# Kernel tuning notes

Hardware: AMD Instinct MI355X
Metric: run time of the kernel (lower is better)

The kernel has to match this reference:

```python
import jax, jax.numpy as jnp
import numpy as np

B, L, C, H = 16, 1024, 512, 8
D = C // H
SCALE = D ** -0.5


def setup_inputs() -> dict:
    key = jax.random.key(0)
    ks = jax.random.split(key, 16)
    s = 0.02  # weight init scale
    inp = {
        "query": jax.random.normal(ks[0], (B, L, C), jnp.float32),
        "query_pos": jax.random.normal(ks[1], (B, L, C), jnp.float32),
        "Wqc": jax.random.normal(ks[2], (C, C), jnp.float32) * s,
        "bqc": jax.random.normal(ks[3], (C,), jnp.float32) * s,
        "Wqp": jax.random.normal(ks[4], (C, C), jnp.float32) * s,
        "bqp": jax.random.normal(ks[5], (C,), jnp.float32) * s,
        "Wkc": jax.random.normal(ks[6], (C, C), jnp.float32) * s,
        "bkc": jax.random.normal(ks[7], (C,), jnp.float32) * s,
        "Wkp": jax.random.normal(ks[8], (C, C), jnp.float32) * s,
        "bkp": jax.random.normal(ks[9], (C,), jnp.float32) * s,
        "Wv": jax.random.normal(ks[10], (C, C), jnp.float32) * s,
        "bv": jax.random.normal(ks[11], (C,), jnp.float32) * s,
        "Wo": jax.random.normal(ks[12], (C, C), jnp.float32) * s,
        "bo": jax.random.normal(ks[13], (C,), jnp.float32) * s,
    }
    return inp


def reference(query, query_pos, Wqc, bqc, Wqp, bqp, Wkc, bkc, Wkp, bkp, Wv, bv, Wo, bo):
    # key = query, value = key, identity = query, key_pos = query_pos (shapes match)
    qc = query @ Wqc.T + bqc          # [B, L, C]
    qp = query_pos @ Wqp.T + bqp
    kc = query @ Wkc.T + bkc
    kp = query_pos @ Wkp.T + bkp
    v = query @ Wv.T + bv

    def split_heads(x):  # [B, L, C] -> [B, H, L, D]
        return x.reshape(B, L, H, D).transpose(0, 2, 1, 3)

    q = split_heads(qc + qp) * SCALE
    k = split_heads(kc + kp)
    vh = split_heads(v)

    attn = jnp.einsum("bhqd,bhkd->bhqk", q, k)
    attn = jax.nn.softmax(attn, axis=-1)
    out = jnp.einsum("bhqk,bhkd->bhqd", attn, vh)  # [B, H, L, D]
    out = out.transpose(0, 2, 1, 3).reshape(B, L, C)
    out = out @ Wo.T + bo
    return query + out
```

## Files before the change

kernel.cpp:

```cpp
#include <hip/hip_runtime.h>

typedef __attribute__((ext_vector_type(8))) short short8;
typedef __attribute__((ext_vector_type(4))) short short4v;
typedef __attribute__((ext_vector_type(4))) float f32x4;
typedef unsigned short u16;

#define QSCALE 0.18033688011112042f

#define BB 16
#define LL 1024
#define CC 512
#define HH 8
#define DD 64
#define MROWS (BB*LL)
#define KPROJ 1024
#define NPROJ 1536

#define WS_XCAT   0ull
#define WS_WCAT   (WS_XCAT + (size_t)MROWS*KPROJ*2)
#define WS_WO     (WS_WCAT + (size_t)NPROJ*KPROJ*2)
#define WS_BIAS   (WS_WO   + (size_t)CC*CC*2)
#define WS_QH     (WS_BIAS + 8192)
#define WS_KH     (WS_QH + (size_t)MROWS*CC*2)
#define WS_VT     (WS_KH + (size_t)MROWS*CC*2)
#define WS_OH     (WS_VT + (size_t)MROWS*CC*2)
#define WS_END    (WS_OH + (size_t)MROWS*CC*2)

__device__ inline short f2bf(float f) {
  unsigned u = __builtin_bit_cast(unsigned, f);
  u = (u + 0x7FFFu + ((u >> 16) & 1u)) >> 16;
  return (short)u;
}

__device__ inline short8 pack8(const float* src) {
  float4 a = ((const float4*)src)[0];
  float4 b = ((const float4*)src)[1];
  short8 v;
  v[0]=f2bf(a.x); v[1]=f2bf(a.y); v[2]=f2bf(a.z); v[3]=f2bf(a.w);
  v[4]=f2bf(b.x); v[5]=f2bf(b.y); v[6]=f2bf(b.z); v[7]=f2bf(b.w);
  return v;
}

__device__ inline void gload_lds16(const u16* g, char* lds_byte) {
  __builtin_amdgcn_global_load_lds(
      (const __attribute__((address_space(1))) unsigned int*)g,
      (__attribute__((address_space(3))) unsigned int*)lds_byte,
      16, 0, 0);
}

__global__ __launch_bounds__(256) void pack_all_kernel(
    const float* __restrict__ q, const float* __restrict__ qp,
    const float* __restrict__ Wqc, const float* __restrict__ Wqp,
    const float* __restrict__ Wkc, const float* __restrict__ Wkp,
    const float* __restrict__ Wv,  const float* __restrict__ Wo,
    const float* __restrict__ bqc, const float* __restrict__ bqp,
    const float* __restrict__ bkc, const float* __restrict__ bkp,
    const float* __restrict__ bv,
    u16* __restrict__ xcat, u16* __restrict__ wcat, u16* __restrict__ wo_bf,
    float* __restrict__ bias_cat) {
  if (blockIdx.x < 8192) {
    int o = blockIdx.x * 256 + threadIdx.x;
    int row = o >> 7;
    int kk  = (o & 127) << 3;
    const float* src = (kk < 512) ? (q + (size_t)row * 512 + kk)
                                  : (qp + (size_t)row * 512 + (kk - 512));
    short8 v = pack8(src);
    *(short8*)(xcat + (size_t)row * KPROJ + kk) = v;
    return;
  }
  int o = (blockIdx.x - 8192) * 256 + threadIdx.x;
  if (o < 196608) {
    int j = o >> 7;
    int kk = (o & 127) << 3;
    const float* src = nullptr;
    if (j < 512)        src = (kk < 512) ? Wqc + (size_t)j * 512 + kk : Wqp + (size_t)j * 512 + (kk - 512);
    else if (j < 1024) { int jj = j - 512;  src = (kk < 512) ? Wkc + (size_t)jj * 512 + kk : Wkp + (size_t)jj * 512 + (kk - 512); }
    else               { int jj = j - 1024; src = (kk < 512) ? Wv  + (size_t)jj * 512 + kk : nullptr; }
    short8 v = {0,0,0,0,0,0,0,0};
    if (src) v = pack8(src);
    *(short8*)(wcat + (size_t)j * KPROJ + kk) = v;
  } else if (o < 229376) {
    int o2 = o - 196608;
    int j = o2 >> 6;
    int kk = (o2 & 63) << 3;
    short8 v = pack8(Wo + (size_t)j * 512 + kk);
    *(short8*)(wo_bf + (size_t)j * 512 + kk) = v;
  }
  if (o < 1536) {
    float v;
    if (o < 512)       v = bqc[o] + bqp[o];
    else if (o < 1024) v = bkc[o - 512] + bkp[o - 512];
    else               v = bv[o - 1024];
    bias_cat[o] = v;
  }
}

template <int KDIM>
__device__ inline void gemm128_loop(const u16* __restrict__ A, const u16* __restrict__ Bw,
                                    int m0, int n0, int nt, u16* lds, f32x4 (&acc)[4][4]) {
  const int tid = threadIdx.x;
  const int lane = tid & 63, wave = tid >> 6;
  const int wr = wave >> 1, wc = wave & 1;
  const int lr = lane & 15, lg = lane >> 4;

  auto stage = [&](int buf, int t) {
    int k0 = t * 64;
    #pragma unroll
    for (int i = 0; i < 4; ++i) {
      int s = i * 256 + tid;
      int row = s >> 3, col = s & 7;
      int colp = col ^ (row & 7);
      gload_lds16(A + (size_t)(m0 + row) * KDIM + k0 + colp * 8,
                  (char*)lds + (size_t)buf * 32768 + (size_t)(i * 256 + wave * 64) * 16);
      gload_lds16(Bw + (size_t)(n0 + row) * KDIM + k0 + colp * 8,
                  (char*)lds + (size_t)buf * 32768 + 16384 + (size_t)(i * 256 + wave * 64) * 16);
    }
  };

  auto rdA = [&](int buf, int mf, int ks) {
    int rowl = wr * 64 + mf * 16 + lr;
    int ch = (ks * 4 + lg) ^ (rowl & 7);
    return *(const short8*)(lds + (size_t)buf * 16384 + (size_t)rowl * 64 + ch * 8);
  };
  auto rdB = [&](int buf, int nf, int ks) {
    int rowl = wc * 64 + nf * 16 + lr;
    int ch = (ks * 4 + lg) ^ (rowl & 7);
    return *(const short8*)(lds + (size_t)buf * 16384 + 8192 + (size_t)rowl * 64 + ch * 8);
  };

  stage(0, 0);
  asm volatile("s_waitcnt vmcnt(0)" ::: "memory");
  __builtin_amdgcn_s_barrier();

  int cur = 0;
  for (int t = 0; t < nt; ++t) {
    if (t + 1 < nt) stage(cur ^ 1, t + 1);
    short8 bf[4][2], af[4][2];
    #pragma unroll
    for (int nf = 0; nf < 4; ++nf)
      #pragma unroll
      for (int ks = 0; ks < 2; ++ks) bf[nf][ks] = rdB(cur, nf, ks);
    #pragma unroll
    for (int mf = 0; mf < 4; ++mf)
      #pragma unroll
      for (int ks = 0; ks < 2; ++ks) af[mf][ks] = rdA(cur, mf, ks);
    __builtin_amdgcn_s_setprio(1);
    #pragma unroll
    for (int mf = 0; mf < 4; ++mf)
      #pragma unroll
      for (int nf = 0; nf < 4; ++nf)
        #pragma unroll
        for (int ks = 0; ks < 2; ++ks)
          acc[mf][nf] = __builtin_amdgcn_mfma_f32_16x16x32_bf16(
              bf[nf][ks], af[mf][ks], acc[mf][nf], 0, 0, 0);
    __builtin_amdgcn_s_setprio(0);
    asm volatile("s_waitcnt vmcnt(0)" ::: "memory");
    __builtin_amdgcn_s_barrier();
    cur ^= 1;
  }
}

__global__ __launch_bounds__(256, 2) void proj_gemm_kernel(
    const u16* __restrict__ Xcat, const u16* __restrict__ Wcat,
    const float* __restrict__ bias_cat,
    u16* __restrict__ Qh, u16* __restrict__ Kh, u16* __restrict__ Vt) {
  __shared__ __align__(16) u16 lds[2 * 16384];

  int id0 = blockIdx.x;
  int swz = (id0 & 7) * 192 + (id0 >> 3);
  int bx = swz / 12, by = swz % 12;
  const int m0 = bx * 128, n0 = by * 128;

  const int tid = threadIdx.x;
  const int lane = tid & 63, wave = tid >> 6;
  const int wr = wave >> 1, wc = wave & 1;
  const int lr = lane & 15, lg = lane >> 4;

  f32x4 acc[4][4];
  f32x4 z4 = {0.f, 0.f, 0.f, 0.f};
  #pragma unroll
  for (int mf = 0; mf < 4; ++mf)
    #pragma unroll
    for (int nf = 0; nf < 4; ++nf) acc[mf][nf] = z4;

  const int nt = (n0 >= 1024) ? 8 : 16;
  gemm128_loop<KPROJ>(Xcat, Wcat, m0, n0, nt, lds, acc);

  if (n0 < 1024) {
    const int cbase = n0 + wc * 64 + lg * 4;
    #pragma unroll
    for (int mf = 0; mf < 4; ++mf) {
      int lglob = m0 + wr * 64 + mf * 16 + lr;
      int bidx = lglob >> 10, lrow = lglob & 1023;
      #pragma unroll
      for (int nf = 0; nf < 4; ++nf) {
        int c = cbase + nf * 16;
        float4 bb = *(const float4*)&bias_cat[c];
        int sec = c >> 9, cj = c & 511;
        int h = cj >> 6, d0 = cj & 63;
        size_t idx = ((size_t)(bidx * HH + h) * LL + lrow) * DD + d0;
        float v0 = acc[mf][nf][0] + bb.x;
        float v1 = acc[mf][nf][1] + bb.y;
        float v2 = acc[mf][nf][2] + bb.z;
        float v3 = acc[mf][nf][3] + bb.w;
        if (sec == 0) { v0 *= QSCALE; v1 *= QSCALE; v2 *= QSCALE; v3 *= QSCALE; }
        short4v o;
        o[0] = f2bf(v0); o[1] = f2bf(v1); o[2] = f2bf(v2); o[3] = f2bf(v3);
        u16* dst = (sec == 0) ? Qh : Kh;
        *(short4v*)&dst[idx] = o;
      }
    }
  } else {
    u16* T = lds;
    #pragma unroll
    for (int mf = 0; mf < 4; ++mf) {
      int ll = wr * 64 + mf * 16 + lr;
      #pragma unroll
      for (int nf = 0; nf < 4; ++nf) {
        int cjl = wc * 64 + nf * 16 + lg * 4;
        int c = n0 + cjl;
        float4 bb = *(const float4*)&bias_cat[c];
        T[(size_t)(cjl + 0) * 136 + ll] = (u16)f2bf(acc[mf][nf][0] + bb.x);
        T[(size_t)(cjl + 1) * 136 + ll] = (u16)f2bf(acc[mf][nf][1] + bb.y);
        T[(size_t)(cjl + 2) * 136 + ll] = (u16)f2bf(acc[mf][nf][2] + bb.z);
        T[(size_t)(cjl + 3) * 136 + ll] = (u16)f2bf(acc[mf][nf][3] + bb.w);
      }
    }
    __builtin_amdgcn_s_barrier();
    int b = m0 >> 10, lrow0 = m0 & 1023;
    #pragma unroll
    for (int i = 0; i < 8; ++i) {
      int c2 = i * 256 + tid;
      int r = c2 >> 4;
      int o8 = (c2 & 15) * 8;
      short8 v = *(const short8*)&T[(size_t)r * 136 + o8];
      int cj = n0 - 1024 + r;
      int h = cj >> 6, d = cj & 63;
      *(short8*)&Vt[((size_t)(b * HH + h) * DD + d) * LL + lrow0 + o8] = v;
    }
  }
}

__global__ __launch_bounds__(256, 2) void out_gemm_kernel(
    const u16* __restrict__ Oh, const u16* __restrict__ Wo_bf,
    const float* __restrict__ bo, const float* __restrict__ query,
    float* __restrict__ out) {
  __shared__ __align__(16) u16 lds[2 * 16384];

  int id0 = blockIdx.x;
  int swz = (id0 & 7) * 64 + (id0 >> 3);
  int bx = swz / 4, by = swz % 4;
  const int m0 = bx * 128, n0 = by * 128;

  const int lane = threadIdx.x & 63, wave = threadIdx.x >> 6;
  const int wr = wave >> 1, wc = wave & 1;
  const int lr = lane & 15, lg = lane >> 4;

  f32x4 acc[4][4];
  f32x4 z4 = {0.f, 0.f, 0.f, 0.f};
  #pragma unroll
  for (int mf = 0; mf < 4; ++mf)
    #pragma unroll
    for (int nf = 0; nf < 4; ++nf) acc[mf][nf] = z4;

  gemm128_loop<CC>(Oh, Wo_bf, m0, n0, CC / 64, lds, acc);

  const int cbase = n0 + wc * 64 + lg * 4;
  #pragma unroll
  for (int mf = 0; mf < 4; ++mf) {
    int rw = m0 + wr * 64 + mf * 16 + lr;
    #pragma unroll
    for (int nf = 0; nf < 4; ++nf) {
      int c = cbase + nf * 16;
      float4 bb = *(const float4*)&bo[c];
      size_t idx = (size_t)rw * CC + c;
      float4 qq = *(const float4*)&query[idx];
      float4 o;
      o.x = acc[mf][nf][0] + bb.x + qq.x;
      o.y = acc[mf][nf][1] + bb.y + qq.y;
      o.z = acc[mf][nf][2] + bb.z + qq.z;
      o.w = acc[mf][nf][3] + bb.w + qq.w;
      *(float4*)&out[idx] = o;
    }
  }
}

__global__ __launch_bounds__(256, 2) void attn_kernel(
    const u16* __restrict__ Qh, const u16* __restrict__ Kh,
    const u16* __restrict__ Vt, u16* __restrict__ Oh) {
  __shared__ __align__(16) u16 Kl[2][64 * 64];
  __shared__ __align__(16) u16 Vl[2][64 * 64];
  __shared__ __align__(16) char Pp[4][8192];

  const int tid = threadIdx.x;
  const int lane = tid & 63, wave = tid >> 6;
  const int lr = lane & 15, lg = lane >> 4;
  const int sw = (lr & 7) * 2;
  int n = blockIdx.x;
  int rest = n >> 3;
  const int bh = (n & 7) * 16 + (rest >> 2);
  const int q0 = (rest & 3) * 256;

  const u16* Qb = Qh + (size_t)bh * LL * DD;
  const u16* Kb = Kh + (size_t)bh * LL * DD;
  const u16* Vb = Vt + (size_t)bh * DD * LL;

  short8 aq[4][2];
  #pragma unroll
  for (int m = 0; m < 4; ++m)
    #pragma unroll
    for (int s = 0; s < 2; ++s)
      aq[m][s] = *(const short8*)(Qb + (size_t)(q0 + wave * 64 + m * 16 + lr) * DD + s * 32 + lg * 8);

  f32x4 z4 = {0.f, 0.f, 0.f, 0.f};
  f32x4 oaccT[4][4];
  #pragma unroll
  for (int m = 0; m < 4; ++m)
    #pragma unroll
    for (int db = 0; db < 4; ++db) oaccT[m][db] = z4;
  float lsums[4] = {0.f, 0.f, 0.f, 0.f};

  auto stage = [&](int buf, int kt) {
    int kk0 = kt * 64;
    #pragma unroll
    for (int i = 0; i < 2; ++i) {
      int c = i * 256 + wave * 64 + lane;
      int row = c >> 3, koct = c & 7;
      int ks = koct ^ (row & 7);
      gload_lds16(Kb + (size_t)(kk0 + row) * DD + ks * 8,
                  (char*)&Kl[buf][0] + (size_t)(i * 4 + wave) * 1024);
      gload_lds16(Vb + (size_t)row * LL + kk0 + ks * 8,
                  (char*)&Vl[buf][0] + (size_t)(i * 4 + wave) * 1024);
    }
  };

  stage(0, 0);
  int cur = 0;
  char* Pw = &Pp[wave][0];
  for (int kt = 0; kt < 16; ++kt) {
    if (kt + 1 < 16) {
      stage(cur ^ 1, kt + 1);
      asm volatile("s_waitcnt vmcnt(4)" ::: "memory");
    } else {
      asm volatile("s_waitcnt vmcnt(0)" ::: "memory");
    }
    __builtin_amdgcn_s_barrier();
    __builtin_amdgcn_sched_barrier(0);

    short8 ka[2][4];
    #pragma unroll
    for (int s = 0; s < 2; ++s)
      #pragma unroll
      for (int kb = 0; kb < 4; ++kb) {
        int key = kb * 16 + lr;
        int dct = s * 4 + lg;
        ka[s][kb] = *(const short8*)((const char*)&Kl[cur][0] + (size_t)key * 128 + ((dct ^ (key & 7)) << 4));
      }
    f32x4 ps[4][4];
    #pragma unroll
    for (int m = 0; m < 4; ++m)
      #pragma unroll
      for (int kb = 0; kb < 4; ++kb) ps[m][kb] = z4;
    __builtin_amdgcn_s_setprio(1);
    #pragma unroll
    for (int s = 0; s < 2; ++s)
      #pragma unroll
      for (int kb = 0; kb < 4; ++kb)
        #pragma unroll
        for (int m = 0; m < 4; ++m)
          ps[m][kb] = __builtin_amdgcn_mfma_f32_16x16x32_bf16(ka[s][kb], aq[m][s], ps[m][kb], 0, 0, 0);
    __builtin_amdgcn_s_setprio(0);

    #pragma unroll
    for (int m = 0; m < 4; ++m) {
      #pragma unroll
      for (int kb = 0; kb < 4; ++kb) {
        float p0, p1, p2, p3;
        asm("v_exp_f32 %0, %1" : "=v"(p0) : "v"(ps[m][kb][0]));
        asm("v_exp_f32 %0, %1" : "=v"(p1) : "v"(ps[m][kb][1]));
        asm("v_exp_f32 %0, %1" : "=v"(p2) : "v"(ps[m][kb][2]));
        asm("v_exp_f32 %0, %1" : "=v"(p3) : "v"(ps[m][kb][3]));
        lsums[m] += (p0 + p1) + (p2 + p3);
        unsigned lo, hi;
        asm("v_cvt_pk_bf16_f32 %0, %1, %2" : "=v"(lo) : "v"(p0), "v"(p1));
        asm("v_cvt_pk_bf16_f32 %0, %1, %2" : "=v"(hi) : "v"(p2), "v"(p3));
        uint2 w; w.x = lo; w.y = hi;
        *(uint2*)(Pw + m * 2048 + lr * 128 + ((((kb * 4 + lg) ^ sw)) << 3)) = w;
      }
    }

    short8 bv[2][4];
    #pragma unroll
    for (int s = 0; s < 2; ++s)
      #pragma unroll
      for (int db = 0; db < 4; ++db) {
        int d = db * 16 + lr;
        int kct = s * 4 + lg;
        bv[s][db] = *(const short8*)((const char*)&Vl[cur][0] + (size_t)d * 128 + ((kct ^ (d & 7)) << 4));
      }

    asm volatile("s_waitcnt lgkmcnt(0)" ::: "memory");
    __builtin_amdgcn_sched_barrier(0);

    __builtin_amdgcn_s_setprio(1);
    #pragma unroll
    for (int m = 0; m < 4; ++m) {
      #pragma unroll
      for (int s = 0; s < 2; ++s) {
        int val0 = s * 8 + lg * 2;
        uint4 pw = *(const uint4*)(Pw + m * 2048 + lr * 128 + (((val0 ^ sw)) << 3));
        short8 ap = __builtin_bit_cast(short8, pw);
        #pragma unroll
        for (int db = 0; db < 4; ++db)
          oaccT[m][db] = __builtin_amdgcn_mfma_f32_16x16x32_bf16(bv[s][db], ap, oaccT[m][db], 0, 0, 0);
      }
    }
    __builtin_amdgcn_s_setprio(0);

    __builtin_amdgcn_s_barrier();
    cur ^= 1;
  }

  int b = bh >> 3, h = bh & 7;
  #pragma unroll
  for (int m = 0; m < 4; ++m) {
    float v = lsums[m];
    v += __shfl_xor(v, 16);
    v += __shfl_xor(v, 32);
    float inv = 1.0f / v;
    int q = q0 + wave * 64 + m * 16 + lr;
    #pragma unroll
    for (int db = 0; db < 4; ++db) {
      int d0 = db * 16 + lg * 4;
      short4v o;
      #pragma unroll
      for (int r = 0; r < 4; ++r) o[r] = f2bf(oaccT[m][db][r] * inv);
      *(short4v*)&Oh[(size_t)(b * LL + q) * CC + h * 64 + d0] = o;
    }
  }
}

extern "C" void kernel_launch(void* const* d_in, const int* in_sizes, int n_in,
                              void* d_out, int out_size, void* d_ws, size_t ws_size,
                              hipStream_t stream) {
  (void)in_sizes; (void)n_in; (void)out_size;
  const float* query = (const float*)d_in[0];
  const float* qpos  = (const float*)d_in[1];
  const float* Wqc = (const float*)d_in[2];
  const float* bqc = (const float*)d_in[3];
  const float* Wqp = (const float*)d_in[4];
  const float* bqp = (const float*)d_in[5];
  const float* Wkc = (const float*)d_in[6];
  const float* bkc = (const float*)d_in[7];
  const float* Wkp = (const float*)d_in[8];
  const float* bkp = (const float*)d_in[9];
  const float* Wv  = (const float*)d_in[10];
  const float* bv  = (const float*)d_in[11];
  const float* Wo  = (const float*)d_in[12];
  const float* bo  = (const float*)d_in[13];

  char* ws = (char*)d_ws;
  if (ws_size < WS_END) return;

  u16*   Xcat     = (u16*)(ws + WS_XCAT);
  u16*   Wcat     = (u16*)(ws + WS_WCAT);
  u16*   Wo_bf    = (u16*)(ws + WS_WO);
  float* bias_cat = (float*)(ws + WS_BIAS);
  u16*   Qh       = (u16*)(ws + WS_QH);
  u16*   Kh       = (u16*)(ws + WS_KH);
  u16*   Vtr      = (u16*)(ws + WS_VT);
  u16*   Oh       = (u16*)(ws + WS_OH);
  float* out      = (float*)d_out;

  pack_all_kernel<<<dim3(9088), dim3(256), 0, stream>>>(
      query, qpos, Wqc, Wqp, Wkc, Wkp, Wv, Wo,
      bqc, bqp, bkc, bkp, bv, Xcat, Wcat, Wo_bf, bias_cat);
  proj_gemm_kernel<<<dim3((MROWS / 128) * (NPROJ / 128)), dim3(256), 0, stream>>>(
      Xcat, Wcat, bias_cat, Qh, Kh, Vtr);
  attn_kernel<<<dim3(512), dim3(256), 0, stream>>>(Qh, Kh, Vtr, Oh);
  out_gemm_kernel<<<dim3((MROWS / 128) * (CC / 128)), dim3(256), 0, stream>>>(
      Oh, Wo_bf, bo, query, out);
}
```

Baseline: 145.4 us.

## Halve GEMM K-tile to 32 and raise occupancy to four blocks per CU

```diff
diff --git a/kernel.cpp b/kernel.cpp
--- a/kernel.cpp
+++ b/kernel.cpp
@@ -104,28 +104,28 @@
   const int lr = lane & 15, lg = lane >> 4;
 
   auto stage = [&](int buf, int t) {
-    int k0 = t * 64;
-    #pragma unroll
-    for (int i = 0; i < 4; ++i) {
+    int k0 = t * 32;
+    #pragma unroll
+    for (int i = 0; i < 2; ++i) {
       int s = i * 256 + tid;
-      int row = s >> 3, col = s & 7;
-      int colp = col ^ (row & 7);
+      int row = s >> 2, col = s & 3;
+      int colp = col ^ (row & 3);
       gload_lds16(A + (size_t)(m0 + row) * KDIM + k0 + colp * 8,
-                  (char*)lds + (size_t)buf * 32768 + (size_t)(i * 256 + wave * 64) * 16);
+                  (char*)lds + (size_t)buf * 16384 + (size_t)(i * 256 + wave * 64) * 16);
       gload_lds16(Bw + (size_t)(n0 + row) * KDIM + k0 + colp * 8,
-                  (char*)lds + (size_t)buf * 32768 + 16384 + (size_t)(i * 256 + wave * 64) * 16);
+                  (char*)lds + (size_t)buf * 16384 + 8192 + (size_t)(i * 256 + wave * 64) * 16);
     }
   };
 
-  auto rdA = [&](int buf, int mf, int ks) {
+  auto rdA = [&](int buf, int mf) {
     int rowl = wr * 64 + mf * 16 + lr;
-    int ch = (ks * 4 + lg) ^ (rowl & 7);
-    return *(const short8*)(lds + (size_t)buf * 16384 + (size_t)rowl * 64 + ch * 8);
+    int ch = lg ^ (rowl & 3);
+    return *(const short8*)(lds + (size_t)buf * 8192 + (size_t)rowl * 32 + ch * 8);
   };
-  auto rdB = [&](int buf, int nf, int ks) {
+  auto rdB = [&](int buf, int nf) {
     int rowl = wc * 64 + nf * 16 + lr;
-    int ch = (ks * 4 + lg) ^ (rowl & 7);
-    return *(const short8*)(lds + (size_t)buf * 16384 + 8192 + (size_t)rowl * 64 + ch * 8);
+    int ch = lg ^ (rowl & 3);
+    return *(const short8*)(lds + (size_t)buf * 8192 + 4096 + (size_t)rowl * 32 + ch * 8);
   };
 
   stage(0, 0);
@@ -135,24 +135,18 @@
   int cur = 0;
   for (int t = 0; t < nt; ++t) {
     if (t + 1 < nt) stage(cur ^ 1, t + 1);
-    short8 bf[4][2], af[4][2];
-    #pragma unroll
-    for (int nf = 0; nf < 4; ++nf)
-      #pragma unroll
-      for (int ks = 0; ks < 2; ++ks) bf[nf][ks] = rdB(cur, nf, ks);
+    short8 bf[4], af[4];
+    #pragma unroll
+    for (int nf = 0; nf < 4; ++nf) bf[nf] = rdB(cur, nf);
+    #pragma unroll
+    for (int mf = 0; mf < 4; ++mf) af[mf] = rdA(cur, mf);
+    __builtin_amdgcn_s_setprio(1);
     #pragma unroll
     for (int mf = 0; mf < 4; ++mf)
       #pragma unroll
-      for (int ks = 0; ks < 2; ++ks) af[mf][ks] = rdA(cur, mf, ks);
-    __builtin_amdgcn_s_setprio(1);
-    #pragma unroll
-    for (int mf = 0; mf < 4; ++mf)
-      #pragma unroll
       for (int nf = 0; nf < 4; ++nf)
-        #pragma unroll
-        for (int ks = 0; ks < 2; ++ks)
-          acc[mf][nf] = __builtin_amdgcn_mfma_f32_16x16x32_bf16(
-              bf[nf][ks], af[mf][ks], acc[mf][nf], 0, 0, 0);
+        acc[mf][nf] = __builtin_amdgcn_mfma_f32_16x16x32_bf16(
+            bf[nf], af[mf], acc[mf][nf], 0, 0, 0);
     __builtin_amdgcn_s_setprio(0);
     asm volatile("s_waitcnt vmcnt(0)" ::: "memory");
     __builtin_amdgcn_s_barrier();
@@ -160,11 +154,11 @@
   }
 }
 
-__global__ __launch_bounds__(256, 2) void proj_gemm_kernel(
+__global__ __launch_bounds__(256, 4) void proj_gemm_kernel(
     const u16* __restrict__ Xcat, const u16* __restrict__ Wcat,
     const float* __restrict__ bias_cat,
     u16* __restrict__ Qh, u16* __restrict__ Kh, u16* __restrict__ Vt) {
-  __shared__ __align__(16) u16 lds[2 * 16384];
+  __shared__ __align__(16) u16 lds[2 * 8192];
 
   int id0 = blockIdx.x;
   int swz = (id0 & 7) * 192 + (id0 >> 3);
@@ -183,7 +177,7 @@
     #pragma unroll
     for (int nf = 0; nf < 4; ++nf) acc[mf][nf] = z4;
 
-  const int nt = (n0 >= 1024) ? 8 : 16;
+  const int nt = (n0 >= 1024) ? 16 : 32;
   gemm128_loop<KPROJ>(Xcat, Wcat, m0, n0, nt, lds, acc);
 
   if (n0 < 1024) {
@@ -212,40 +206,46 @@
     }
   } else {
     u16* T = lds;
-    #pragma unroll
-    for (int mf = 0; mf < 4; ++mf) {
-      int ll = wr * 64 + mf * 16 + lr;
-      #pragma unroll
-      for (int nf = 0; nf < 4; ++nf) {
-        int cjl = wc * 64 + nf * 16 + lg * 4;
-        int c = n0 + cjl;
-        float4 bb = *(const float4*)&bias_cat[c];
-        T[(size_t)(cjl + 0) * 136 + ll] = (u16)f2bf(acc[mf][nf][0] + bb.x);
-        T[(size_t)(cjl + 1) * 136 + ll] = (u16)f2bf(acc[mf][nf][1] + bb.y);
-        T[(size_t)(cjl + 2) * 136 + ll] = (u16)f2bf(acc[mf][nf][2] + bb.z);
-        T[(size_t)(cjl + 3) * 136 + ll] = (u16)f2bf(acc[mf][nf][3] + bb.w);
-      }
-    }
-    __builtin_amdgcn_s_barrier();
     int b = m0 >> 10, lrow0 = m0 & 1023;
     #pragma unroll
-    for (int i = 0; i < 8; ++i) {
-      int c2 = i * 256 + tid;
-      int r = c2 >> 4;
-      int o8 = (c2 & 15) * 8;
-      short8 v = *(const short8*)&T[(size_t)r * 136 + o8];
-      int cj = n0 - 1024 + r;
-      int h = cj >> 6, d = cj & 63;
-      *(short8*)&Vt[((size_t)(b * HH + h) * DD + d) * LL + lrow0 + o8] = v;
-    }
-  }
-}
-
-__global__ __launch_bounds__(256, 2) void out_gemm_kernel(
+    for (int p = 0; p < 2; ++p) {
+      if (wc == p) {
+        #pragma unroll
+        for (int mf = 0; mf < 4; ++mf) {
+          int ll = wr * 64 + mf * 16 + lr;
+          #pragma unroll
+          for (int nf = 0; nf < 4; ++nf) {
+            int cjl = nf * 16 + lg * 4;
+            int c = n0 + p * 64 + cjl;
+            float4 bb = *(const float4*)&bias_cat[c];
+            T[(size_t)(cjl + 0) * 136 + ll] = (u16)f2bf(acc[mf][nf][0] + bb.x);
+            T[(size_t)(cjl + 1) * 136 + ll] = (u16)f2bf(acc[mf][nf][1] + bb.y);
+            T[(size_t)(cjl + 2) * 136 + ll] = (u16)f2bf(acc[mf][nf][2] + bb.z);
+            T[(size_t)(cjl + 3) * 136 + ll] = (u16)f2bf(acc[mf][nf][3] + bb.w);
+          }
+        }
+      }
+      __builtin_amdgcn_s_barrier();
+      #pragma unroll
+      for (int i = 0; i < 4; ++i) {
+        int c2 = i * 256 + tid;
+        int r = c2 >> 4;
+        int o8 = (c2 & 15) * 8;
+        short8 v = *(const short8*)&T[(size_t)r * 136 + o8];
+        int cj = n0 - 1024 + p * 64 + r;
+        int h = cj >> 6, d = cj & 63;
+        *(short8*)&Vt[((size_t)(b * HH + h) * DD + d) * LL + lrow0 + o8] = v;
+      }
+      __builtin_amdgcn_s_barrier();
+    }
+  }
+}
+
+__global__ __launch_bounds__(256, 4) void out_gemm_kernel(
     const u16* __restrict__ Oh, const u16* __restrict__ Wo_bf,
     const float* __restrict__ bo, const float* __restrict__ query,
     float* __restrict__ out) {
-  __shared__ __align__(16) u16 lds[2 * 16384];
+  __shared__ __align__(16) u16 lds[2 * 8192];
 
   int id0 = blockIdx.x;
   int swz = (id0 & 7) * 64 + (id0 >> 3);
@@ -263,7 +263,7 @@
     #pragma unroll
     for (int nf = 0; nf < 4; ++nf) acc[mf][nf] = z4;
 
-  gemm128_loop<CC>(Oh, Wo_bf, m0, n0, CC / 64, lds, acc);
+  gemm128_loop<CC>(Oh, Wo_bf, m0, n0, CC / 32, lds, acc);
 
   const int cbase = n0 + wc * 64 + lg * 4;
   #pragma unroll
```

After: 147.4 us. Within noise of the previous version (+1.4%).
